# Optimization experiments

Hardware: AMD Instinct MI355X
Metric: run time of the kernel (lower is better)

The kernel has to match this reference:

```python
import jax, jax.numpy as jnp
import numpy as np

DMODEL = 1024
HEADS = 16
HEAD_SIZE = DMODEL // HEADS


def setup_inputs() -> dict:
    key = jax.random.key(0)
    ks = jax.random.split(key, 9)
    s = 1.0 / np.sqrt(DMODEL)
    x = jax.random.normal(ks[0], (4, 2048, DMODEL), dtype=jnp.float32)
    Wq = jax.random.uniform(ks[1], (DMODEL, DMODEL), jnp.float32, -s, s)
    bq = jax.random.uniform(ks[2], (DMODEL,), jnp.float32, -s, s)
    Wk = jax.random.uniform(ks[3], (DMODEL, DMODEL), jnp.float32, -s, s)
    bk = jax.random.uniform(ks[4], (DMODEL,), jnp.float32, -s, s)
    Wv = jax.random.uniform(ks[5], (DMODEL, DMODEL), jnp.float32, -s, s)
    bv = jax.random.uniform(ks[6], (DMODEL,), jnp.float32, -s, s)
    Wo = jax.random.uniform(ks[7], (DMODEL, DMODEL), jnp.float32, -s, s)
    bo = jax.random.uniform(ks[8], (DMODEL,), jnp.float32, -s, s)
    return {"x": x, "Wq": Wq, "bq": bq, "Wk": Wk, "bk": bk,
            "Wv": Wv, "bv": bv, "Wo": Wo, "bo": bo}


def _split_heads(t):
    b, s, _ = t.shape
    return t.reshape(b, s, HEADS, HEAD_SIZE).transpose(0, 2, 1, 3)  # [b,h,s,d]


def reference(x, Wq, bq, Wk, bk, Wv, bv, Wo, bo):
    q = _split_heads(x @ Wq.T + bq)
    k = _split_heads(x @ Wk.T + bk)
    v = _split_heads(x @ Wv.T + bv)
    scale = 1.0 / jnp.sqrt(jnp.float32(HEAD_SIZE))
    scores = jnp.einsum("bhqd,bhkd->bhqk", q, k) * scale  # full [B,H,S,S]
    attn = jax.nn.softmax(scores, axis=-1)
    out = jnp.einsum("bhqk,bhkd->bhqd", attn, v)
    b, h, s, d = out.shape
    out = out.transpose(0, 2, 1, 3).reshape(b, s, h * d)
    return out @ Wo.T + bo
```

## Files before the change

### kernel.cpp

```cpp
#include <hip/hip_runtime.h>

typedef _Float16 f16x8 __attribute__((ext_vector_type(8)));
typedef _Float16 f16x4 __attribute__((ext_vector_type(4)));
typedef _Float16 f16x2 __attribute__((ext_vector_type(2)));
typedef float f32x4 __attribute__((ext_vector_type(4)));

#define MFMA16(a, b, c) __builtin_amdgcn_mfma_f32_16x16x32_f16(a, b, c, 0, 0, 0)

static constexpr int DM   = 1024;
static constexpr int SEQ  = 2048;
static constexpr int NHEAD = 16;
static constexpr int HD   = 64;

__device__ __forceinline__ void gload16(const _Float16* g, _Float16* l) {
  __builtin_amdgcn_global_load_lds((const __attribute__((address_space(1))) void*)g,
                                   (__attribute__((address_space(3))) void*)l, 16, 0, 0);
}

__global__ __launch_bounds__(256) void cvt_kernel(
    const float* __restrict__ x,  const float* __restrict__ wq,
    const float* __restrict__ wk, const float* __restrict__ wv,
    const float* __restrict__ wo, _Float16* __restrict__ dst)
{
  const int NX4 = 2097152;
  const int NW4 = 262144;
  const int total = NX4 + 4 * NW4;
  for (int i = blockIdx.x * blockDim.x + threadIdx.x; i < total;
       i += gridDim.x * blockDim.x) {
    const float* src; size_t doff; int off;
    if (i < NX4) { src = x; off = i; doff = (size_t)i * 4; }
    else {
      int j = i - NX4; int wi = j >> 18; off = j & (NW4 - 1);
      src = wi == 0 ? wq : wi == 1 ? wk : wi == 2 ? wv : wo;
      doff = 8388608u + (size_t)wi * 1048576u + (size_t)off * 4;
    }
    f32x4 v = *(const f32x4*)(src + (size_t)off * 4);
    f16x4 hh;
    hh[0] = (_Float16)v[0]; hh[1] = (_Float16)v[1];
    hh[2] = (_Float16)v[2]; hh[3] = (_Float16)v[3];
    *(f16x4*)(dst + doff) = hh;
  }
}

__device__ __forceinline__ void gemm_core(
    const _Float16* __restrict__ Abase, const _Float16* __restrict__ Bbase,
    int K, _Float16* As, _Float16* Bs, int w, int l, int wr, int wc,
    f32x4 acc[4][4])
{
  const int l15 = l & 15, lg = l >> 4;
  const int r4 = l >> 2, kq = (l & 3) * 8;
  for (int k0 = 0; k0 < K; k0 += 32) {
    #pragma unroll
    for (int c = 0; c < 2; c++) {
      int row = c * 64 + w * 16 + r4;
      gload16(Abase + (size_t)row * K + k0 + kq, As + c * 2048 + w * 512 + l * 8);
      gload16(Bbase + (size_t)row * K + k0 + kq, Bs + c * 2048 + w * 512 + l * 8);
    }
    __syncthreads();
    f16x8 af[4], bfr[4];
    #pragma unroll
    for (int mt = 0; mt < 4; mt++)
      af[mt] = *(const f16x8*)(As + (wr * 64 + mt * 16 + l15) * 32 + lg * 8);
    #pragma unroll
    for (int nt = 0; nt < 4; nt++)
      bfr[nt] = *(const f16x8*)(Bs + (wc * 64 + nt * 16 + l15) * 32 + lg * 8);
    #pragma unroll
    for (int mt = 0; mt < 4; mt++)
      #pragma unroll
      for (int nt = 0; nt < 4; nt++)
        acc[mt][nt] = MFMA16(af[mt], bfr[nt], acc[mt][nt]);
    __syncthreads();
  }
}

__global__ __launch_bounds__(256) void qkv_gemm(
    const _Float16* __restrict__ xh,
    const _Float16* __restrict__ wqh, const _Float16* __restrict__ wkh,
    const _Float16* __restrict__ wvh,
    const float* __restrict__ bq, const float* __restrict__ bk,
    const float* __restrict__ bv,
    _Float16* __restrict__ qo, _Float16* __restrict__ ko,
    _Float16* __restrict__ vto)
{
  __shared__ __attribute__((aligned(16))) _Float16 As[4096], Bs[4096];
  const int tid = threadIdx.x, w = tid >> 6, l = tid & 63;
  const int l15 = l & 15, lg = l >> 4;
  const int wr = w >> 1, wc = w & 1;
  const int bx = blockIdx.x;
  const int sel = bx >> 3;
  const int n0 = (bx & 7) * 128;
  const int m0 = blockIdx.y * 128;
  const _Float16* W = sel == 0 ? wqh : sel == 1 ? wkh : wvh;
  const float* bias = sel == 0 ? bq : sel == 1 ? bk : bv;

  f32x4 acc[4][4] = {};
  gemm_core(xh + (size_t)m0 * DM, W + (size_t)n0 * DM, DM, As, Bs, w, l, wr, wc, acc);

  float biasv[4];
  #pragma unroll
  for (int nt = 0; nt < 4; nt++) biasv[nt] = bias[n0 + wc * 64 + nt * 16 + l15];

  if (sel < 2) {
    _Float16* outp = sel == 0 ? qo : ko;
    #pragma unroll
    for (int mt = 0; mt < 4; mt++) {
      int row = m0 + wr * 64 + mt * 16 + lg * 4;
      #pragma unroll
      for (int nt = 0; nt < 4; nt++) {
        int col = n0 + wc * 64 + nt * 16 + l15;
        #pragma unroll
        for (int r = 0; r < 4; r++)
          outp[(size_t)(row + r) * DM + col] = (_Float16)(acc[mt][nt][r] + biasv[nt]);
      }
    }
  } else {
    #pragma unroll
    for (int mt = 0; mt < 4; mt++) {
      int row0 = m0 + wr * 64 + mt * 16 + lg * 4;
      int b = row0 >> 11, s0 = row0 & 2047;
      #pragma unroll
      for (int nt = 0; nt < 4; nt++) {
        int col = n0 + wc * 64 + nt * 16 + l15;
        int hh = col >> 6, d = col & 63;
        f16x4 pk;
        #pragma unroll
        for (int r = 0; r < 4; r++) pk[r] = (_Float16)(acc[mt][nt][r] + biasv[nt]);
        *(f16x4*)(vto + ((size_t)((b * NHEAD + hh) * HD + d)) * SEQ + s0) = pk;
      }
    }
  }
}

__global__ __launch_bounds__(256, 3) void attn_kernel(
    const _Float16* __restrict__ qh, const _Float16* __restrict__ kh,
    const _Float16* __restrict__ vth, _Float16* __restrict__ atth)
{
  __shared__ __attribute__((aligned(16))) _Float16 Ks[2][4096];
  __shared__ __attribute__((aligned(16))) _Float16 Vs[2][4096];

  const int gid = blockIdx.x;
  const int bh = gid & 63, qt = gid >> 6;
  const int b = bh >> 4, h = bh & 15;
  const int tid = threadIdx.x, w = tid >> 6, l = tid & 63;
  const int l15 = l & 15, lg = l >> 4;
  const int q0 = qt * 128 + w * 32;

  const float c2 = 0.125f * 1.4426950408889634f;
  const _Float16 hc2 = (_Float16)c2;

  const _Float16* qbase = qh + (size_t)(b * SEQ + q0) * DM + h * HD;
  f16x8 aq[2][2];
  #pragma unroll
  for (int g = 0; g < 2; g++)
    #pragma unroll
    for (int ks = 0; ks < 2; ks++) {
      f16x8 v = *(const f16x8*)(qbase + (size_t)(g * 16 + l15) * DM + ks * 32 + lg * 8);
      #pragma unroll
      for (int j = 0; j < 8; j++) v[j] *= hc2;
      aq[g][ks] = v;
    }

  const _Float16* kbase = kh + (size_t)b * SEQ * DM + h * HD;
  const _Float16* vbase = vth + (size_t)bh * HD * SEQ;

  const int s0 = w * 64 + l, s1 = 256 + s0;
  const int kr0 = s0 >> 3, kc0 = (s0 & 7) ^ (kr0 & 7);
  const int kr1 = s1 >> 3, kc1 = (s1 & 7) ^ (kr1 & 7);

  f32x4 o[2][4] = {};
  f32x4 lr[2] = {};
  f16x8 ones;
  #pragma unroll
  for (int j = 0; j < 8; j++) ones[j] = (_Float16)1.0f;

  gload16(kbase + (size_t)kr0 * DM + kc0 * 8, &Ks[0][s0 * 8]);
  gload16(kbase + (size_t)kr1 * DM + kc1 * 8, &Ks[0][s1 * 8]);
  gload16(vbase + (size_t)kr0 * SEQ + kc0 * 8, &Vs[0][s0 * 8]);
  gload16(vbase + (size_t)kr1 * SEQ + kc1 * 8, &Vs[0][s1 * 8]);

  for (int t = 0; t < 32; t++) {
    const int cur = t & 1;
    if (t < 31) {
      const int kv1 = (t + 1) * 64;
      gload16(kbase + (size_t)(kv1 + kr0) * DM + kc0 * 8, &Ks[cur ^ 1][s0 * 8]);
      gload16(kbase + (size_t)(kv1 + kr1) * DM + kc1 * 8, &Ks[cur ^ 1][s1 * 8]);
      gload16(vbase + (size_t)kr0 * SEQ + kv1 + kc0 * 8, &Vs[cur ^ 1][s0 * 8]);
      gload16(vbase + (size_t)kr1 * SEQ + kv1 + kc1 * 8, &Vs[cur ^ 1][s1 * 8]);
      asm volatile("s_waitcnt vmcnt(4)" ::: "memory");
    } else {
      asm volatile("s_waitcnt vmcnt(0)" ::: "memory");
    }
    __builtin_amdgcn_s_barrier();
    asm volatile("" ::: "memory");

    f16x8 bkf[4][2], vf[4][2];
    #pragma unroll
    for (int nt = 0; nt < 4; nt++)
      #pragma unroll
      for (int ks = 0; ks < 2; ks++) {
        const int off = (nt * 16 + l15) * 64 + (((ks * 4 + lg) ^ (l15 & 7)) << 3);
        bkf[nt][ks] = *(const f16x8*)&Ks[cur][off];
        vf[nt][ks]  = *(const f16x8*)&Vs[cur][off];
      }

    f32x4 sc[2][4] = {};
    __builtin_amdgcn_s_setprio(1);
    #pragma unroll
    for (int g = 0; g < 2; g++)
      #pragma unroll
      for (int nt = 0; nt < 4; nt++) {
        sc[g][nt] = MFMA16(bkf[nt][0], aq[g][0], sc[g][nt]);
        sc[g][nt] = MFMA16(bkf[nt][1], aq[g][1], sc[g][nt]);
      }
    __builtin_amdgcn_s_setprio(0);

    #pragma unroll
    for (int g = 0; g < 2; g++) {
      unsigned pkA[4], pkB[4];
      #pragma unroll
      for (int nt = 0; nt < 4; nt++) {
        float e0 = exp2f(sc[g][nt][0]), e1 = exp2f(sc[g][nt][1]);
        float e2 = exp2f(sc[g][nt][2]), e3 = exp2f(sc[g][nt][3]);
        pkA[nt] = __builtin_bit_cast(unsigned, __builtin_amdgcn_cvt_pkrtz(e0, e1));
        pkB[nt] = __builtin_bit_cast(unsigned, __builtin_amdgcn_cvt_pkrtz(e2, e3));
      }
      f16x8 pa[2];
      #pragma unroll
      for (int ks = 0; ks < 2; ks++) {
        unsigned a0 = pkA[2 * ks], a1 = pkA[2 * ks + 1];
        unsigned b0 = pkB[2 * ks], b1 = pkB[2 * ks + 1];
        asm("v_permlane32_swap_b32 %0, %1" : "+v"(a0), "+v"(a1));
        asm("v_permlane16_swap_b32 %0, %1" : "+v"(a0), "+v"(a1));
        asm("v_permlane32_swap_b32 %0, %1" : "+v"(b0), "+v"(b1));
        asm("v_permlane16_swap_b32 %0, %1" : "+v"(b0), "+v"(b1));
        union { unsigned u[4]; f16x8 v; } pk;
        pk.u[0] = a0; pk.u[1] = b0; pk.u[2] = a1; pk.u[3] = b1;
        pa[ks] = pk.v;
      }
      __builtin_amdgcn_s_setprio(1);
      lr[g] = MFMA16(pa[0], ones, lr[g]);
      lr[g] = MFMA16(pa[1], ones, lr[g]);
      #pragma unroll
      for (int nt = 0; nt < 4; nt++) {
        o[g][nt] = MFMA16(pa[0], vf[nt][0], o[g][nt]);
        o[g][nt] = MFMA16(pa[1], vf[nt][1], o[g][nt]);
      }
      __builtin_amdgcn_s_setprio(0);
    }

    asm volatile("s_waitcnt lgkmcnt(0)" ::: "memory");
    __builtin_amdgcn_s_barrier();
    asm volatile("" ::: "memory");
  }

  #pragma unroll
  for (int g = 0; g < 2; g++)
    #pragma unroll
    for (int r = 0; r < 4; r++) {
      float inv = 1.f / lr[g][r];
      int row = q0 + g * 16 + lg * 4 + r;
      #pragma unroll
      for (int nt = 0; nt < 4; nt++)
        atth[(size_t)(b * SEQ + row) * DM + h * HD + nt * 16 + l15] =
            (_Float16)(o[g][nt][r] * inv);
    }
}

__global__ __launch_bounds__(256) void out_gemm(
    const _Float16* __restrict__ ah, const _Float16* __restrict__ woh,
    const float* __restrict__ bo, float* __restrict__ out)
{
  __shared__ __attribute__((aligned(16))) _Float16 As[4096], Bs[4096];
  const int tid = threadIdx.x, w = tid >> 6, l = tid & 63;
  const int l15 = l & 15, lg = l >> 4;
  const int wr = w >> 1, wc = w & 1;
  const int n0 = blockIdx.x * 128;
  const int m0 = blockIdx.y * 128;

  f32x4 acc[4][4] = {};
  gemm_core(ah + (size_t)m0 * DM, woh + (size_t)n0 * DM, DM, As, Bs, w, l, wr, wc, acc);

  float biasv[4];
  #pragma unroll
  for (int nt = 0; nt < 4; nt++) biasv[nt] = bo[n0 + wc * 64 + nt * 16 + l15];
  #pragma unroll
  for (int mt = 0; mt < 4; mt++) {
    int row = m0 + wr * 64 + mt * 16 + lg * 4;
    #pragma unroll
    for (int nt = 0; nt < 4; nt++) {
      int col = n0 + wc * 64 + nt * 16 + l15;
      #pragma unroll
      for (int r = 0; r < 4; r++)
        out[(size_t)(row + r) * DM + col] = acc[mt][nt][r] + biasv[nt];
    }
  }
}

extern "C" void kernel_launch(void* const* d_in, const int* in_sizes, int n_in,
                              void* d_out, int out_size, void* d_ws, size_t ws_size,
                              hipStream_t stream)
{
  const float* x  = (const float*)d_in[0];
  const float* Wq = (const float*)d_in[1];
  const float* bq = (const float*)d_in[2];
  const float* Wk = (const float*)d_in[3];
  const float* bk = (const float*)d_in[4];
  const float* Wv = (const float*)d_in[5];
  const float* bv = (const float*)d_in[6];
  const float* Wo = (const float*)d_in[7];
  const float* bo = (const float*)d_in[8];
  float* out = (float*)d_out;

  _Float16* base = (_Float16*)d_ws;
  _Float16* xh  = base;
  _Float16* wqh = base + 8388608;
  _Float16* wkh = base + 9437184;
  _Float16* wvh = base + 10485760;
  _Float16* woh = base + 11534336;
  _Float16* qhp = base + 12582912;
  _Float16* khp = base + 20971520;
  _Float16* vth = base + 29360128;
  _Float16* ath = xh;

  cvt_kernel<<<1024, 256, 0, stream>>>(x, Wq, Wk, Wv, Wo, base);
  qkv_gemm<<<dim3(24, 64), 256, 0, stream>>>(xh, wqh, wkh, wvh, bq, bk, bv, qhp, khp, vth);
  attn_kernel<<<1024, 256, 0, stream>>>(qhp, khp, vth, ath);
  out_gemm<<<dim3(8, 64), 256, 0, stream>>>(ath, woh, bo, out);
}
```

Measured before the change: 210.6 us.

## Triple-buffer K/V tiles in attention with one barrier per iteration and raw v_exp

The attention kernel now keeps three K/V LDS buffers instead of two and prefetches two tiles ahead. This lets each loop iteration use a single barrier instead of two, which cuts synchronisation stalls and gives global loads more time to land. The exp2f call is also replaced with inline v_exp_f32, dropping the range-handling code the library adds. The cost is 16 KB more LDS per block, which may limit occupancy under launch_bounds(256,3), and raw v_exp may lose accuracy for denormal results.

```diff
diff --git a/kernel.cpp b/kernel.cpp
--- a/kernel.cpp
+++ b/kernel.cpp
@@ -2,7 +2,6 @@
 
 typedef _Float16 f16x8 __attribute__((ext_vector_type(8)));
 typedef _Float16 f16x4 __attribute__((ext_vector_type(4)));
-typedef _Float16 f16x2 __attribute__((ext_vector_type(2)));
 typedef float f32x4 __attribute__((ext_vector_type(4)));
 
 #define MFMA16(a, b, c) __builtin_amdgcn_mfma_f32_16x16x32_f16(a, b, c, 0, 0, 0)
@@ -15,6 +14,10 @@
 __device__ __forceinline__ void gload16(const _Float16* g, _Float16* l) {
   __builtin_amdgcn_global_load_lds((const __attribute__((address_space(1))) void*)g,
                                    (__attribute__((address_space(3))) void*)l, 16, 0, 0);
+}
+
+__device__ __forceinline__ float fexp2(float x) {
+  float y; asm("v_exp_f32 %0, %1" : "=v"(y) : "v"(x)); return y;
 }
 
 __global__ __launch_bounds__(256) void cvt_kernel(
@@ -135,8 +138,8 @@
     const _Float16* __restrict__ qh, const _Float16* __restrict__ kh,
     const _Float16* __restrict__ vth, _Float16* __restrict__ atth)
 {
-  __shared__ __attribute__((aligned(16))) _Float16 Ks[2][4096];
-  __shared__ __attribute__((aligned(16))) _Float16 Vs[2][4096];
+  __shared__ __attribute__((aligned(16))) _Float16 Ks[3][4096];
+  __shared__ __attribute__((aligned(16))) _Float16 Vs[3][4096];
 
   const int gid = blockIdx.x;
   const int bh = gid & 63, qt = gid >> 6;
@@ -173,34 +176,39 @@
   #pragma unroll
   for (int j = 0; j < 8; j++) ones[j] = (_Float16)1.0f;
 
-  gload16(kbase + (size_t)kr0 * DM + kc0 * 8, &Ks[0][s0 * 8]);
-  gload16(kbase + (size_t)kr1 * DM + kc1 * 8, &Ks[0][s1 * 8]);
-  gload16(vbase + (size_t)kr0 * SEQ + kc0 * 8, &Vs[0][s0 * 8]);
-  gload16(vbase + (size_t)kr1 * SEQ + kc1 * 8, &Vs[0][s1 * 8]);
-
+  #pragma unroll
+  for (int t0 = 0; t0 < 2; t0++) {
+    const int kv = t0 * 64;
+    gload16(kbase + (size_t)(kv + kr0) * DM + kc0 * 8, &Ks[t0][s0 * 8]);
+    gload16(kbase + (size_t)(kv + kr1) * DM + kc1 * 8, &Ks[t0][s1 * 8]);
+    gload16(vbase + (size_t)kr0 * SEQ + kv + kc0 * 8, &Vs[t0][s0 * 8]);
+    gload16(vbase + (size_t)kr1 * SEQ + kv + kc1 * 8, &Vs[t0][s1 * 8]);
+  }
+  asm volatile("s_waitcnt vmcnt(4)" ::: "memory");
+
+  int cur = 0, pre = 2;
   for (int t = 0; t < 32; t++) {
-    const int cur = t & 1;
-    if (t < 31) {
-      const int kv1 = (t + 1) * 64;
-      gload16(kbase + (size_t)(kv1 + kr0) * DM + kc0 * 8, &Ks[cur ^ 1][s0 * 8]);
-      gload16(kbase + (size_t)(kv1 + kr1) * DM + kc1 * 8, &Ks[cur ^ 1][s1 * 8]);
-      gload16(vbase + (size_t)kr0 * SEQ + kv1 + kc0 * 8, &Vs[cur ^ 1][s0 * 8]);
-      gload16(vbase + (size_t)kr1 * SEQ + kv1 + kc1 * 8, &Vs[cur ^ 1][s1 * 8]);
-      asm volatile("s_waitcnt vmcnt(4)" ::: "memory");
-    } else {
-      asm volatile("s_waitcnt vmcnt(0)" ::: "memory");
-    }
     __builtin_amdgcn_s_barrier();
     asm volatile("" ::: "memory");
 
+    if (t < 30) {
+      const int kv2 = (t + 2) * 64;
+      gload16(kbase + (size_t)(kv2 + kr0) * DM + kc0 * 8, &Ks[pre][s0 * 8]);
+      gload16(kbase + (size_t)(kv2 + kr1) * DM + kc1 * 8, &Ks[pre][s1 * 8]);
+      gload16(vbase + (size_t)kr0 * SEQ + kv2 + kc0 * 8, &Vs[pre][s0 * 8]);
+      gload16(vbase + (size_t)kr1 * SEQ + kv2 + kc1 * 8, &Vs[pre][s1 * 8]);
+    }
+
+    const _Float16* kb = &Ks[cur][0];
+    const _Float16* vb = &Vs[cur][0];
     f16x8 bkf[4][2], vf[4][2];
     #pragma unroll
     for (int nt = 0; nt < 4; nt++)
       #pragma unroll
       for (int ks = 0; ks < 2; ks++) {
         const int off = (nt * 16 + l15) * 64 + (((ks * 4 + lg) ^ (l15 & 7)) << 3);
-        bkf[nt][ks] = *(const f16x8*)&Ks[cur][off];
-        vf[nt][ks]  = *(const f16x8*)&Vs[cur][off];
+        bkf[nt][ks] = *(const f16x8*)&kb[off];
+        vf[nt][ks]  = *(const f16x8*)&vb[off];
       }
 
     f32x4 sc[2][4] = {};
@@ -219,8 +227,8 @@
       unsigned pkA[4], pkB[4];
       #pragma unroll
       for (int nt = 0; nt < 4; nt++) {
-        float e0 = exp2f(sc[g][nt][0]), e1 = exp2f(sc[g][nt][1]);
-        float e2 = exp2f(sc[g][nt][2]), e3 = exp2f(sc[g][nt][3]);
+        float e0 = fexp2(sc[g][nt][0]), e1 = fexp2(sc[g][nt][1]);
+        float e2 = fexp2(sc[g][nt][2]), e3 = fexp2(sc[g][nt][3]);
         pkA[nt] = __builtin_bit_cast(unsigned, __builtin_amdgcn_cvt_pkrtz(e0, e1));
         pkB[nt] = __builtin_bit_cast(unsigned, __builtin_amdgcn_cvt_pkrtz(e2, e3));
       }
@@ -248,9 +256,14 @@
       __builtin_amdgcn_s_setprio(0);
     }
 
-    asm volatile("s_waitcnt lgkmcnt(0)" ::: "memory");
-    __builtin_amdgcn_s_barrier();
-    asm volatile("" ::: "memory");
+    if (t < 31) {
+      asm volatile("s_waitcnt lgkmcnt(0)" ::: "memory");
+      if (t < 30) asm volatile("s_waitcnt vmcnt(4)" ::: "memory");
+      else        asm volatile("s_waitcnt vmcnt(0)" ::: "memory");
+      __builtin_amdgcn_sched_barrier(0);
+    }
+    cur = cur == 2 ? 0 : cur + 1;
+    pre = pre == 2 ? 0 : pre + 1;
   }
 
   #pragma unroll
```

Measured after the change: 187.5 us. -11.0%, faster.
